# Optimization experiments

Hardware: AMD Instinct MI355X
Metric: run time of the kernel (lower is better)

## Reference

```python
import jax, jax.numpy as jnp
import numpy as np

MASK_LOGIT_CONST = 1000000000.0
LN_EPS = 1e-12


def setup_inputs() -> dict:
    key = jax.random.key(0)
    k_in, k_w = jax.random.split(key)
    B, S, H = 8, 2048, 1024
    inputs = jax.random.normal(k_in, (B, S, H), dtype=jnp.float32)
    masks = jnp.ones((B, S, S), dtype=jnp.float32)
    w_match = jax.random.normal(k_w, (2 * H, H), dtype=jnp.float32) * (1.0 / np.sqrt(2 * H))
    b_match = jnp.zeros((H,), dtype=jnp.float32)
    ln_gamma = jnp.ones((H,), dtype=jnp.float32)
    ln_beta = jnp.zeros((H,), dtype=jnp.float32)
    return {"inputs": inputs, "masks": masks, "w_match": w_match,
            "b_match": b_match, "ln_gamma": ln_gamma, "ln_beta": ln_beta}


def reference(inputs, masks, w_match, b_match, ln_gamma, ln_beta):
    H = inputs.shape[-1]
    scale = 1.0 / jnp.sqrt(jnp.asarray(H, dtype=inputs.dtype))
    # self-attention scores [B,S,S] (dropout disabled -> query=key=inputs)
    scores = jnp.einsum('bsh,bth->bst', inputs, inputs) * scale
    # logits_mask: scores*mask + (-C)*(1-mask)
    scores = scores * masks - MASK_LOGIT_CONST * (1.0 - masks)
    probs = jax.nn.softmax(scores, axis=-1)
    context = jnp.einsum('bst,bth->bsh', probs, inputs)
    cat = jnp.concatenate([inputs, context], axis=-1)  # [B,S,2H]
    matching = jnp.einsum('bsk,kh->bsh', cat, w_match) + b_match
    # layernorm over last dim
    mu = jnp.mean(matching, axis=-1, keepdims=True)
    var = jnp.mean((matching - mu) ** 2, axis=-1, keepdims=True)
    normed = (matching - mu) * jax.lax.rsqrt(var + LN_EPS)
    return normed * ln_gamma + ln_beta
```

## Files before the change

### kernel.cpp

```cpp
#include <hip/hip_runtime.h>
#include <hip/hip_bf16.h>
#include <hip/hip_fp8.h>


typedef unsigned short ushort_t;
typedef __attribute__((ext_vector_type(8))) short short8;
typedef __attribute__((ext_vector_type(4))) float float4v;

__device__ inline float b2f(unsigned int u) {
    union { unsigned int i; float f; } v; v.i = u << 16; return v.f;
}
__device__ inline ushort_t f2b(float f) {
    __hip_bfloat16 h = __float2bfloat16(f);
    return __builtin_bit_cast(ushort_t, h);
}
__device__ inline unsigned char f2e4(float f) {
    return __hip_fp8_e4m3(f).__x;
}

__device__ inline void gload_lds16(const void* g, void* lds) {
    __builtin_amdgcn_global_load_lds(
        (const __attribute__((address_space(1))) unsigned int*)g,
        (__attribute__((address_space(3))) unsigned int*)lds, 16, 0, 0);
}

template<int EPI>
__global__ __launch_bounds__(512, 2)
void gemm_bt(const ushort_t* __restrict__ A, const ushort_t* __restrict__ A2, int kSplit,
             const ushort_t* __restrict__ B,
             int M, int N, int K, int lda, int ldb, int ldc,
             long aBS, long bBS, long cBS,
             const float* __restrict__ rowsum,
             const float* __restrict__ bias,
             ushort_t* __restrict__ outb)
{
    __shared__ __align__(16) ushort_t smem[4 * 16384];

    const int tid = threadIdx.x;
    const int z = blockIdx.z;
    A  += (size_t)z * aBS;
    A2 += (size_t)z * aBS;
    B  += (size_t)z * bBS;
    if (EPI == 2) rowsum += (size_t)z * M;
    outb += (size_t)z * cBS;

    const int bm = blockIdx.x * 256;
    const int bn = blockIdx.y * 256;
    const int w = tid >> 6, lane = tid & 63;
    const int wm = (w >> 2) * 128, wn = (w & 3) * 64;
    const int q = lane >> 4, l15 = lane & 15;
    const int srow = lane >> 2;
    const int schunk = ((lane & 3) ^ ((lane >> 3) & 3)) * 8;

    float4v acc[8][4];
#pragma unroll
    for (int i = 0; i < 8; i++)
#pragma unroll
        for (int j = 0; j < 4; j++) acc[i][j] = (float4v){0.f, 0.f, 0.f, 0.f};

    const int NT = K >> 5;

#define STAGE(T) do {                                                               \
        const int k0_ = (T) * 32;                                                   \
        const ushort_t* aS_ = A; int ka_ = k0_;                                     \
        if (k0_ >= kSplit) { aS_ = A2; ka_ = k0_ - kSplit; }                        \
        ushort_t* buf_ = &smem[((T) & 3) * 16384];                                  \
        gload_lds16(aS_ + (size_t)(bm + w * 16       + srow) * lda + ka_ + schunk,  \
                    buf_ + w * 512);                                                \
        gload_lds16(aS_ + (size_t)(bm + (w + 8) * 16 + srow) * lda + ka_ + schunk,  \
                    buf_ + (w + 8) * 512);                                          \
        gload_lds16(B   + (size_t)(bn + w * 16       + srow) * ldb + k0_ + schunk,  \
                    buf_ + 8192 + w * 512);                                         \
        gload_lds16(B   + (size_t)(bn + (w + 8) * 16 + srow) * ldb + k0_ + schunk,  \
                    buf_ + 8192 + (w + 8) * 512);                                   \
    } while (0)

    STAGE(0); STAGE(1); STAGE(2);

    for (int T = 0; T < NT; ++T) {
        if (T + 2 < NT)      asm volatile("s_waitcnt vmcnt(8)\n\ts_barrier" ::: "memory");
        else if (T + 1 < NT) asm volatile("s_waitcnt vmcnt(4)\n\ts_barrier" ::: "memory");
        else                 asm volatile("s_waitcnt vmcnt(0)\n\ts_barrier" ::: "memory");

        if (T + 3 < NT) STAGE(T + 3);

        const ushort_t* bufA = &smem[(T & 3) * 16384];
        const ushort_t* bufB = bufA + 8192;
        short8 af[8], bf[4];
#pragma unroll
        for (int mi = 0; mi < 8; mi++) {
            const int r = wm + mi * 16 + l15;
            af[mi] = *(const short8*)(&bufA[r * 32 + ((q ^ ((r >> 1) & 3)) << 3)]);
        }
#pragma unroll
        for (int ni = 0; ni < 4; ni++) {
            const int r = wn + ni * 16 + l15;
            bf[ni] = *(const short8*)(&bufB[r * 32 + ((q ^ ((r >> 1) & 3)) << 3)]);
        }
        __builtin_amdgcn_s_setprio(1);
#pragma unroll
        for (int mi = 0; mi < 8; mi++)
#pragma unroll
            for (int ni = 0; ni < 4; ni++)
                acc[mi][ni] = __builtin_amdgcn_mfma_f32_16x16x32_bf16(
                    af[mi], bf[ni], acc[mi][ni], 0, 0, 0);
        __builtin_amdgcn_s_setprio(0);
    }
#undef STAGE

#pragma unroll
    for (int mi = 0; mi < 8; mi++) {
#pragma unroll
        for (int r = 0; r < 4; r++) {
            const int row = bm + wm + mi * 16 + q * 4 + r;
            const size_t ro = (size_t)row * ldc;
            float rsinv = 1.f;
            if (EPI == 2) rsinv = 1.0f / rowsum[row];
#pragma unroll
            for (int ni = 0; ni < 4; ni++) {
                const int col = bn + wn + ni * 16 + l15;
                float v = acc[mi][ni][r];
                if (EPI == 2) outb[ro + col] = f2b(v * rsinv);
                else          outb[ro + col] = f2b(v + bias[col]);
            }
        }
    }
}

__global__ __launch_bounds__(256, 2)
void gemm1_fp8(const unsigned char* __restrict__ X8,
               const float* __restrict__ mask,
               float* __restrict__ rowsum,
               ushort_t* __restrict__ E)
{
    __shared__ __align__(16) unsigned char As[128 * 128];
    __shared__ __align__(16) unsigned char Bs[128 * 128];

    const int tid = threadIdx.x;
    const int z = blockIdx.z;
    const unsigned char* Xz = X8 + (size_t)z * 2048 * 1024;
    const float* mz = mask + (size_t)z * 2048 * 2048;
    float* rsz = rowsum + (size_t)z * 2048;
    ushort_t* Ez = E + (size_t)z * 2048 * 2048;

    const int bm = blockIdx.x * 128;
    const int bn = blockIdx.y * 128;
    const int wave = tid >> 6, lane = tid & 63;
    const int wm = (wave >> 1) * 64, wn = (wave & 1) * 64;
    const int q = lane >> 4, l15 = lane & 15;
    const int rx = l15 & 7;
    const int lrow = lane >> 3;
    const int cswz = (lane & 7) ^ lrow;

    float4v acc[4][4];
#pragma unroll
    for (int i = 0; i < 4; i++)
#pragma unroll
        for (int j = 0; j < 4; j++) acc[i][j] = (float4v){0.f, 0.f, 0.f, 0.f};

    for (int k0 = 0; k0 < 1024; k0 += 128) {
#pragma unroll
        for (int j = 0; j < 4; j++) {
            const int p = wave * 4 + j;
            const int ro = p * 8 + lrow;
            gload_lds16(Xz + (size_t)(bm + ro) * 1024 + k0 + cswz * 16, &As[p * 1024]);
            gload_lds16(Xz + (size_t)(bn + ro) * 1024 + k0 + cswz * 16, &Bs[p * 1024]);
        }
        __syncthreads();
#pragma unroll
        for (int kk = 0; kk < 128; kk += 32) {
            const int g = (kk >> 3) + q;
            const int co = (((g >> 1) ^ rx) << 4) + ((g & 1) << 3);
            long af[4], bfv[4];
#pragma unroll
            for (int mi = 0; mi < 4; mi++)
                af[mi] = *(const long*)(&As[(wm + mi * 16 + l15) * 128 + co]);
#pragma unroll
            for (int ni = 0; ni < 4; ni++)
                bfv[ni] = *(const long*)(&Bs[(wn + ni * 16 + l15) * 128 + co]);
#pragma unroll
            for (int mi = 0; mi < 4; mi++)
#pragma unroll
                for (int ni = 0; ni < 4; ni++)
                    acc[mi][ni] = __builtin_amdgcn_mfma_f32_16x16x32_fp8_fp8(
                        af[mi], bfv[ni], acc[mi][ni], 0, 0, 0);
        }
        __syncthreads();
    }

    const float scale = 0.03125f;
#pragma unroll
    for (int mi = 0; mi < 4; mi++) {
#pragma unroll
        for (int r = 0; r < 4; r++) {
            const int row = bm + wm + mi * 16 + q * 4 + r;
            const size_t ro = (size_t)row * 2048;
            float s = 0.f;
#pragma unroll
            for (int ni = 0; ni < 4; ni++) {
                const int col = bn + wn + ni * 16 + l15;
                const float m = mz[ro + col];
                float v = __expf(acc[mi][ni][r] * scale * m - 1e9f * (1.0f - m));
                s += v;
                Ez[ro + col] = f2b(v);
            }
            s += __shfl_xor(s, 8);
            s += __shfl_xor(s, 4);
            s += __shfl_xor(s, 2);
            s += __shfl_xor(s, 1);
            if (l15 == 0) atomicAdd(&rsz[row], s);
        }
    }
}

__global__ __launch_bounds__(256)
void conv_trans(const float* __restrict__ in, ushort_t* __restrict__ outT,
                ushort_t* __restrict__ outS, unsigned char* __restrict__ outQ,
                int R, int C)
{
    __shared__ float tile[64][65];
    const int tx = threadIdx.x & 15, ty = threadIdx.x >> 4;
    const size_t zoff = (size_t)blockIdx.z * R * C;
    const int r0 = blockIdx.y * 64, c0 = blockIdx.x * 64;
#pragma unroll
    for (int j = 0; j < 4; j++) {
        const int r = ty + j * 16;
        const float4 v = *(const float4*)(in + zoff + (size_t)(r0 + r) * C + c0 + tx * 4);
        tile[r][tx * 4 + 0] = v.x;
        tile[r][tx * 4 + 1] = v.y;
        tile[r][tx * 4 + 2] = v.z;
        tile[r][tx * 4 + 3] = v.w;
        if (outS) {
            ushort4 o;
            o.x = f2b(v.x); o.y = f2b(v.y); o.z = f2b(v.z); o.w = f2b(v.w);
            *(ushort4*)(outS + zoff + (size_t)(r0 + r) * C + c0 + tx * 4) = o;
            uchar4 p;
            p.x = f2e4(v.x); p.y = f2e4(v.y); p.z = f2e4(v.z); p.w = f2e4(v.w);
            *(uchar4*)(outQ + zoff + (size_t)(r0 + r) * C + c0 + tx * 4) = p;
        }
    }
    __syncthreads();
    ushort_t* tp = outT + zoff;
#pragma unroll
    for (int j = 0; j < 4; j++) {
        const int cc = ty + j * 16;
        ushort4 o;
        o.x = f2b(tile[tx * 4 + 0][cc]);
        o.y = f2b(tile[tx * 4 + 1][cc]);
        o.z = f2b(tile[tx * 4 + 2][cc]);
        o.w = f2b(tile[tx * 4 + 3][cc]);
        *(ushort4*)(tp + (size_t)(c0 + cc) * R + r0 + tx * 4) = o;
    }
}

__global__ __launch_bounds__(256)
void ln_k(const ushort_t* __restrict__ Mt, const float* __restrict__ gamma,
          const float* __restrict__ beta, float* __restrict__ out)
{
    const size_t row = blockIdx.x;
    const int tid = threadIdx.x;
    const ushort4 u = *(const ushort4*)(Mt + row * 1024 + tid * 4);
    float x0 = b2f(u.x), x1 = b2f(u.y), x2 = b2f(u.z), x3 = b2f(u.w);
    float s  = x0 + x1 + x2 + x3;
    float s2 = x0 * x0 + x1 * x1 + x2 * x2 + x3 * x3;
#pragma unroll
    for (int off = 32; off > 0; off >>= 1) {
        s  += __shfl_down(s, off);
        s2 += __shfl_down(s2, off);
    }
    __shared__ float red[8];
    const int wave = tid >> 6, lane = tid & 63;
    if (lane == 0) { red[wave] = s; red[4 + wave] = s2; }
    __syncthreads();
    s  = red[0] + red[1] + red[2] + red[3];
    s2 = red[4] + red[5] + red[6] + red[7];
    const float mu  = s * (1.0f / 1024.0f);
    const float var = s2 * (1.0f / 1024.0f) - mu * mu;
    const float rinv = rsqrtf(var + 1e-12f);
    const float4 g = *(const float4*)(gamma + tid * 4);
    const float4 b = *(const float4*)(beta + tid * 4);
    float4 o;
    o.x = (x0 - mu) * rinv * g.x + b.x;
    o.y = (x1 - mu) * rinv * g.y + b.y;
    o.z = (x2 - mu) * rinv * g.z + b.z;
    o.w = (x3 - mu) * rinv * g.w + b.w;
    *(float4*)(out + row * 1024 + tid * 4) = o;
}

extern "C" void kernel_launch(void* const* d_in, const int* in_sizes, int n_in,
                              void* d_out, int out_size, void* d_ws, size_t ws_size,
                              hipStream_t stream)
{
    const float* X     = (const float*)d_in[0];
    const float* masks = (const float*)d_in[1];
    const float* Wm    = (const float*)d_in[2];
    const float* bias  = (const float*)d_in[3];
    const float* gamma = (const float*)d_in[4];
    const float* beta  = (const float*)d_in[5];
    float* out = (float*)d_out;
    char* ws = (char*)d_ws;

    const int B = 8, S = 2048, H = 1024;

    ushort_t* Xb  = (ushort_t*)(ws);
    ushort_t* XT  = (ushort_t*)(ws + 33554432);
    ushort_t* WT  = (ushort_t*)(ws + 67108864);
    ushort_t* E   = (ushort_t*)(ws + 71303168);
    float*    rs  = (float*)   (ws + 138412032);
    ushort_t* CTX = (ushort_t*)(ws + 138477568);
    unsigned char* X8 = (unsigned char*)CTX;
    ushort_t* matching = E;

    conv_trans<<<dim3(16, 32, 8), 256, 0, stream>>>(X, XT, Xb, X8, S, H);
    conv_trans<<<dim3(16, 32, 1), 256, 0, stream>>>(Wm, WT, nullptr, nullptr, 2 * H, H);
    hipMemsetAsync(rs, 0, (size_t)B * S * sizeof(float), stream);

    gemm1_fp8<<<dim3(16, 16, 8), 256, 0, stream>>>(X8, masks, rs, E);

    gemm_bt<2><<<dim3(8, 4, 8), 512, 0, stream>>>(
        E, E, 1 << 30, XT,
        S, H, S, S, S, H,
        (long)S * S, (long)H * S, (long)S * H,
        rs, nullptr, CTX);

    gemm_bt<3><<<dim3(64, 4, 1), 512, 0, stream>>>(
        Xb, CTX, H, WT,
        B * S, H, 2 * H, H, 2 * H, H,
        0, 0, 0,
        nullptr, bias, matching);

    ln_k<<<B * S, 256, 0, stream>>>(matching, gamma, beta, out);
}
```

Measured before the change: 480.8 us.

## Enlarge FP8 score GEMM tile and add four-stage LDS prefetch pipeline

The FP8 QK^T score kernel now computes 256x256 tiles with 8 waves, each owning a 128x64 sub-tile. The K loop uses 64-wide chunks in a 4-buffer LDS ring, keeping three stages in flight through explicit vmcnt waits and a single barrier per step, and raises wave priority around the MFMA block. This aims to hide global-load latency and raise operand reuse per LDS byte. In exchange it uses 128KB of LDS, so likely only one block fits per CU despite the launch bound of 2, and doubles accumulator registers per wave.

```diff
diff --git a/kernel.cpp b/kernel.cpp
--- a/kernel.cpp
+++ b/kernel.cpp
@@ -6,6 +6,7 @@
 typedef unsigned short ushort_t;
 typedef __attribute__((ext_vector_type(8))) short short8;
 typedef __attribute__((ext_vector_type(4))) float float4v;
+typedef __attribute__((ext_vector_type(2))) long long2v;
 
 __device__ inline float b2f(unsigned int u) {
     union { unsigned int i; float f; } v; v.i = u << 16; return v.f;
@@ -127,14 +128,13 @@
     }
 }
 
-__global__ __launch_bounds__(256, 2)
+__global__ __launch_bounds__(512, 2)
 void gemm1_fp8(const unsigned char* __restrict__ X8,
                const float* __restrict__ mask,
                float* __restrict__ rowsum,
                ushort_t* __restrict__ E)
 {
-    __shared__ __align__(16) unsigned char As[128 * 128];
-    __shared__ __align__(16) unsigned char Bs[128 * 128];
+    __shared__ __align__(16) unsigned char smem[4 * 32768];
 
     const int tid = threadIdx.x;
     const int z = blockIdx.z;
@@ -143,54 +143,71 @@
     float* rsz = rowsum + (size_t)z * 2048;
     ushort_t* Ez = E + (size_t)z * 2048 * 2048;
 
-    const int bm = blockIdx.x * 128;
-    const int bn = blockIdx.y * 128;
-    const int wave = tid >> 6, lane = tid & 63;
-    const int wm = (wave >> 1) * 64, wn = (wave & 1) * 64;
+    const int bm = blockIdx.x * 256;
+    const int bn = blockIdx.y * 256;
+    const int w = tid >> 6, lane = tid & 63;
+    const int wm = (w >> 2) * 128, wn = (w & 3) * 64;
     const int q = lane >> 4, l15 = lane & 15;
-    const int rx = l15 & 7;
-    const int lrow = lane >> 3;
-    const int cswz = (lane & 7) ^ lrow;
-
-    float4v acc[4][4];
-#pragma unroll
-    for (int i = 0; i < 4; i++)
+    const int srow = lane >> 2;
+    const int schunk = ((lane & 3) ^ ((lane >> 3) & 3)) * 16;
+
+    float4v acc[8][4];
+#pragma unroll
+    for (int i = 0; i < 8; i++)
 #pragma unroll
         for (int j = 0; j < 4; j++) acc[i][j] = (float4v){0.f, 0.f, 0.f, 0.f};
 
-    for (int k0 = 0; k0 < 1024; k0 += 128) {
-#pragma unroll
-        for (int j = 0; j < 4; j++) {
-            const int p = wave * 4 + j;
-            const int ro = p * 8 + lrow;
-            gload_lds16(Xz + (size_t)(bm + ro) * 1024 + k0 + cswz * 16, &As[p * 1024]);
-            gload_lds16(Xz + (size_t)(bn + ro) * 1024 + k0 + cswz * 16, &Bs[p * 1024]);
-        }
-        __syncthreads();
-#pragma unroll
-        for (int kk = 0; kk < 128; kk += 32) {
-            const int g = (kk >> 3) + q;
-            const int co = (((g >> 1) ^ rx) << 4) + ((g & 1) << 3);
-            long af[4], bfv[4];
-#pragma unroll
-            for (int mi = 0; mi < 4; mi++)
-                af[mi] = *(const long*)(&As[(wm + mi * 16 + l15) * 128 + co]);
-#pragma unroll
-            for (int ni = 0; ni < 4; ni++)
-                bfv[ni] = *(const long*)(&Bs[(wn + ni * 16 + l15) * 128 + co]);
-#pragma unroll
-            for (int mi = 0; mi < 4; mi++)
+#define STAGE1(T) do {                                                                        \
+        const int k0_ = (T) * 64;                                                             \
+        unsigned char* buf_ = &smem[((T) & 3) * 32768];                                       \
+        gload_lds16(Xz + (size_t)(bm + w * 16        + srow) * 1024 + k0_ + schunk,           \
+                    buf_ + w * 1024);                                                         \
+        gload_lds16(Xz + (size_t)(bm + 128 + w * 16  + srow) * 1024 + k0_ + schunk,           \
+                    buf_ + 8192 + w * 1024);                                                  \
+        gload_lds16(Xz + (size_t)(bn + w * 16        + srow) * 1024 + k0_ + schunk,           \
+                    buf_ + 16384 + w * 1024);                                                 \
+        gload_lds16(Xz + (size_t)(bn + 128 + w * 16  + srow) * 1024 + k0_ + schunk,           \
+                    buf_ + 16384 + 8192 + w * 1024);                                          \
+    } while (0)
+
+    STAGE1(0); STAGE1(1); STAGE1(2);
+
+    for (int T = 0; T < 16; ++T) {
+        if (T < 14)      asm volatile("s_waitcnt vmcnt(8)\n\ts_barrier" ::: "memory");
+        else if (T < 15) asm volatile("s_waitcnt vmcnt(4)\n\ts_barrier" ::: "memory");
+        else             asm volatile("s_waitcnt vmcnt(0)\n\ts_barrier" ::: "memory");
+
+        if (T + 3 < 16) STAGE1(T + 3);
+
+        const unsigned char* bufA = &smem[(T & 3) * 32768];
+        const unsigned char* bufB = bufA + 16384;
+        long2v af[8], bf[4];
+#pragma unroll
+        for (int mi = 0; mi < 8; mi++) {
+            const int r = wm + mi * 16 + l15;
+            af[mi] = *(const long2v*)(&bufA[r * 64 + ((q ^ ((r >> 1) & 3)) << 4)]);
+        }
+#pragma unroll
+        for (int ni = 0; ni < 4; ni++) {
+            const int r = wn + ni * 16 + l15;
+            bf[ni] = *(const long2v*)(&bufB[r * 64 + ((q ^ ((r >> 1) & 3)) << 4)]);
+        }
+        __builtin_amdgcn_s_setprio(1);
+#pragma unroll
+        for (int s = 0; s < 2; s++)
+#pragma unroll
+            for (int mi = 0; mi < 8; mi++)
 #pragma unroll
                 for (int ni = 0; ni < 4; ni++)
                     acc[mi][ni] = __builtin_amdgcn_mfma_f32_16x16x32_fp8_fp8(
-                        af[mi], bfv[ni], acc[mi][ni], 0, 0, 0);
-        }
-        __syncthreads();
-    }
+                        af[mi][s], bf[ni][s], acc[mi][ni], 0, 0, 0);
+        __builtin_amdgcn_s_setprio(0);
+    }
+#undef STAGE1
 
     const float scale = 0.03125f;
 #pragma unroll
-    for (int mi = 0; mi < 4; mi++) {
+    for (int mi = 0; mi < 8; mi++) {
 #pragma unroll
         for (int r = 0; r < 4; r++) {
             const int row = bm + wm + mi * 16 + q * 4 + r;
@@ -315,7 +332,7 @@
     conv_trans<<<dim3(16, 32, 1), 256, 0, stream>>>(Wm, WT, nullptr, nullptr, 2 * H, H);
     hipMemsetAsync(rs, 0, (size_t)B * S * sizeof(float), stream);
 
-    gemm1_fp8<<<dim3(16, 16, 8), 256, 0, stream>>>(X8, masks, rs, E);
+    gemm1_fp8<<<dim3(8, 8, 8), 512, 0, stream>>>(X8, masks, rs, E);
 
     gemm_bt<2><<<dim3(8, 4, 8), 512, 0, stream>>>(
         E, E, 1 << 30, XT,
```

Result: slower. 502.4 us (+4.5%).

## Shrink bf16 GEMM tile to 256x128 with double buffering for higher occupancy

Applied to the files above, without the earlier changes.

The shared bf16 GEMM kernel now uses a 256x128 output tile instead of 256x256, and a 2-stage LDS buffer instead of a 4-stage one. Each thread issues 3 async loads per stage, and the wave computes its 128x32 subtile in two halves to keep register use low. Launch bounds rise to 4 blocks per CU and both GEMM launches double their grid in N. The aim is more blocks in flight and better latency hiding on the 256-block grids, at the cost of less data reuse per tile and a shallower prefetch pipeline that waits on all loads every iteration.

```diff
diff --git a/kernel.cpp b/kernel.cpp
--- a/kernel.cpp
+++ b/kernel.cpp
@@ -25,7 +25,7 @@
 }
 
 template<int EPI>
-__global__ __launch_bounds__(512, 2)
+__global__ __launch_bounds__(512, 4)
 void gemm_bt(const ushort_t* __restrict__ A, const ushort_t* __restrict__ A2, int kSplit,
              const ushort_t* __restrict__ B,
              int M, int N, int K, int lda, int ldb, int ldc,
@@ -34,7 +34,7 @@
              const float* __restrict__ bias,
              ushort_t* __restrict__ outb)
 {
-    __shared__ __align__(16) ushort_t smem[4 * 16384];
+    __shared__ __align__(16) ushort_t smem[2 * 12288];
 
     const int tid = threadIdx.x;
     const int z = blockIdx.z;
@@ -45,66 +45,79 @@
     outb += (size_t)z * cBS;
 
     const int bm = blockIdx.x * 256;
-    const int bn = blockIdx.y * 256;
+    const int bn = blockIdx.y * 128;
     const int w = tid >> 6, lane = tid & 63;
-    const int wm = (w >> 2) * 128, wn = (w & 3) * 64;
+    const int wm = (w >> 2) * 128, wn = (w & 3) * 32;
     const int q = lane >> 4, l15 = lane & 15;
-    const int srow = lane >> 2;
-    const int schunk = ((lane & 3) ^ ((lane >> 3) & 3)) * 8;
-
-    float4v acc[8][4];
+    const int srow = tid >> 2;
+    const int schunk = ((tid & 3) ^ ((tid >> 3) & 3)) * 8;
+    const int wbase = w * 512;
+
+    float4v acc[8][2];
 #pragma unroll
     for (int i = 0; i < 8; i++)
 #pragma unroll
-        for (int j = 0; j < 4; j++) acc[i][j] = (float4v){0.f, 0.f, 0.f, 0.f};
+        for (int j = 0; j < 2; j++) acc[i][j] = (float4v){0.f, 0.f, 0.f, 0.f};
 
     const int NT = K >> 5;
 
-#define STAGE(T) do {                                                               \
-        const int k0_ = (T) * 32;                                                   \
-        const ushort_t* aS_ = A; int ka_ = k0_;                                     \
-        if (k0_ >= kSplit) { aS_ = A2; ka_ = k0_ - kSplit; }                        \
-        ushort_t* buf_ = &smem[((T) & 3) * 16384];                                  \
-        gload_lds16(aS_ + (size_t)(bm + w * 16       + srow) * lda + ka_ + schunk,  \
-                    buf_ + w * 512);                                                \
-        gload_lds16(aS_ + (size_t)(bm + (w + 8) * 16 + srow) * lda + ka_ + schunk,  \
-                    buf_ + (w + 8) * 512);                                          \
-        gload_lds16(B   + (size_t)(bn + w * 16       + srow) * ldb + k0_ + schunk,  \
-                    buf_ + 8192 + w * 512);                                         \
-        gload_lds16(B   + (size_t)(bn + (w + 8) * 16 + srow) * ldb + k0_ + schunk,  \
-                    buf_ + 8192 + (w + 8) * 512);                                   \
+#define STAGE(T) do {                                                                \
+        const int k0_ = (T) * 32;                                                    \
+        const ushort_t* aS_ = A; int ka_ = k0_;                                      \
+        if (k0_ >= kSplit) { aS_ = A2; ka_ = k0_ - kSplit; }                         \
+        ushort_t* buf_ = &smem[((T) & 1) * 12288];                                   \
+        gload_lds16(aS_ + (size_t)(bm + srow)       * lda + ka_ + schunk,            \
+                    buf_ + wbase);                                                   \
+        gload_lds16(aS_ + (size_t)(bm + 128 + srow) * lda + ka_ + schunk,            \
+                    buf_ + 4096 + wbase);                                            \
+        gload_lds16(B   + (size_t)(bn + srow)       * ldb + k0_ + schunk,            \
+                    buf_ + 8192 + wbase);                                            \
     } while (0)
 
-    STAGE(0); STAGE(1); STAGE(2);
-
-    for (int T = 0; T < NT; ++T) {
-        if (T + 2 < NT)      asm volatile("s_waitcnt vmcnt(8)\n\ts_barrier" ::: "memory");
-        else if (T + 1 < NT) asm volatile("s_waitcnt vmcnt(4)\n\ts_barrier" ::: "memory");
-        else                 asm volatile("s_waitcnt vmcnt(0)\n\ts_barrier" ::: "memory");
-
-        if (T + 3 < NT) STAGE(T + 3);
-
-        const ushort_t* bufA = &smem[(T & 3) * 16384];
+    STAGE(0);
+    asm volatile("s_waitcnt vmcnt(0)" ::: "memory");
+    __builtin_amdgcn_s_barrier();
+
+    for (int t = 0; t < NT; ++t) {
+        if (t + 1 < NT) STAGE(t + 1);
+
+        const ushort_t* bufA = &smem[(t & 1) * 12288];
         const ushort_t* bufB = bufA + 8192;
-        short8 af[8], bf[4];
-#pragma unroll
-        for (int mi = 0; mi < 8; mi++) {
+        short8 af[4], bf[2];
+#pragma unroll
+        for (int ni = 0; ni < 2; ni++) {
+            const int r = wn + ni * 16 + l15;
+            bf[ni] = *(const short8*)(&bufB[r * 32 + ((q ^ ((r >> 1) & 3)) << 3)]);
+        }
+#pragma unroll
+        for (int mi = 0; mi < 4; mi++) {
             const int r = wm + mi * 16 + l15;
             af[mi] = *(const short8*)(&bufA[r * 32 + ((q ^ ((r >> 1) & 3)) << 3)]);
         }
-#pragma unroll
-        for (int ni = 0; ni < 4; ni++) {
-            const int r = wn + ni * 16 + l15;
-            bf[ni] = *(const short8*)(&bufB[r * 32 + ((q ^ ((r >> 1) & 3)) << 3)]);
-        }
         __builtin_amdgcn_s_setprio(1);
 #pragma unroll
-        for (int mi = 0; mi < 8; mi++)
-#pragma unroll
-            for (int ni = 0; ni < 4; ni++)
+        for (int mi = 0; mi < 4; mi++)
+#pragma unroll
+            for (int ni = 0; ni < 2; ni++)
                 acc[mi][ni] = __builtin_amdgcn_mfma_f32_16x16x32_bf16(
                     af[mi], bf[ni], acc[mi][ni], 0, 0, 0);
         __builtin_amdgcn_s_setprio(0);
+#pragma unroll
+        for (int mi = 0; mi < 4; mi++) {
+            const int r = wm + 64 + mi * 16 + l15;
+            af[mi] = *(const short8*)(&bufA[r * 32 + ((q ^ ((r >> 1) & 3)) << 3)]);
+        }
+        __builtin_amdgcn_s_setprio(1);
+#pragma unroll
+        for (int mi = 0; mi < 4; mi++)
+#pragma unroll
+            for (int ni = 0; ni < 2; ni++)
+                acc[4 + mi][ni] = __builtin_amdgcn_mfma_f32_16x16x32_bf16(
+                    af[mi], bf[ni], acc[4 + mi][ni], 0, 0, 0);
+        __builtin_amdgcn_s_setprio(0);
+
+        asm volatile("s_waitcnt vmcnt(0)" ::: "memory");
+        __builtin_amdgcn_s_barrier();
     }
 #undef STAGE
 
@@ -117,7 +130,7 @@
             float rsinv = 1.f;
             if (EPI == 2) rsinv = 1.0f / rowsum[row];
 #pragma unroll
-            for (int ni = 0; ni < 4; ni++) {
+            for (int ni = 0; ni < 2; ni++) {
                 const int col = bn + wn + ni * 16 + l15;
                 float v = acc[mi][ni][r];
                 if (EPI == 2) outb[ro + col] = f2b(v * rsinv);
@@ -317,13 +330,13 @@
 
     gemm1_fp8<<<dim3(16, 16, 8), 256, 0, stream>>>(X8, masks, rs, E);
 
-    gemm_bt<2><<<dim3(8, 4, 8), 512, 0, stream>>>(
+    gemm_bt<2><<<dim3(8, 8, 8), 512, 0, stream>>>(
         E, E, 1 << 30, XT,
         S, H, S, S, S, H,
         (long)S * S, (long)H * S, (long)S * H,
         rs, nullptr, CTX);
 
-    gemm_bt<3><<<dim3(64, 4, 1), 512, 0, stream>>>(
+    gemm_bt<3><<<dim3(64, 8, 1), 512, 0, stream>>>(
         Xb, CTX, H, WT,
         B * S, H, 2 * H, H, 2 * H, H,
         0, 0, 0,
```

Measured after the change: 500.9 us. 4.2% more time.

## Compute softmax row sums inside PV GEMM and merge conversion launches

Applied to the files above, without the earlier changes.

Softmax denominators are no longer built with atomicAdd in the exp/score kernel. The PV GEMM now sums the bf16 probability fragments it already loads from LDS, reduces them across lanes, and keeps them in shared memory for the normalisation epilogue. This removes the global atomics, the rowsum buffer and its memset. The input and weight transpose/convert kernels are also merged into one launch, using an extra z-slice for the weight. The cost is some extra convert-and-add work inside the GEMM main loop, repeated by every column block.

```diff
diff --git a/kernel.cpp b/kernel.cpp
--- a/kernel.cpp
+++ b/kernel.cpp
@@ -30,7 +30,6 @@
              const ushort_t* __restrict__ B,
              int M, int N, int K, int lda, int ldb, int ldc,
              long aBS, long bBS, long cBS,
-             const float* __restrict__ rowsum,
              const float* __restrict__ bias,
              ushort_t* __restrict__ outb)
 {
@@ -41,7 +40,6 @@
     A  += (size_t)z * aBS;
     A2 += (size_t)z * aBS;
     B  += (size_t)z * bBS;
-    if (EPI == 2) rowsum += (size_t)z * M;
     outb += (size_t)z * cBS;
 
     const int bm = blockIdx.x * 256;
@@ -57,6 +55,8 @@
     for (int i = 0; i < 8; i++)
 #pragma unroll
         for (int j = 0; j < 4; j++) acc[i][j] = (float4v){0.f, 0.f, 0.f, 0.f};
+
+    float rsum0 = 0.f, rsum1 = 0.f;
 
     const int NT = K >> 5;
 
@@ -91,6 +91,12 @@
         for (int mi = 0; mi < 8; mi++) {
             const int r = wm + mi * 16 + l15;
             af[mi] = *(const short8*)(&bufA[r * 32 + ((q ^ ((r >> 1) & 3)) << 3)]);
+            if (EPI == 2 && (mi >> 1) == (w & 3)) {
+                float s8 = 0.f;
+#pragma unroll
+                for (int e = 0; e < 8; e++) s8 += b2f((ushort_t)af[mi][e]);
+                if (mi & 1) rsum1 += s8; else rsum0 += s8;
+            }
         }
 #pragma unroll
         for (int ni = 0; ni < 4; ni++) {
@@ -108,6 +114,18 @@
     }
 #undef STAGE
 
+    float* rsld = (float*)smem;
+    if (EPI == 2) {
+        rsum0 += __shfl_xor(rsum0, 16); rsum0 += __shfl_xor(rsum0, 32);
+        rsum1 += __shfl_xor(rsum1, 16); rsum1 += __shfl_xor(rsum1, 32);
+        if (lane < 16) {
+            const int m0 = 2 * (w & 3);
+            rsld[wm + m0 * 16 + l15]       = rsum0;
+            rsld[wm + (m0 + 1) * 16 + l15] = rsum1;
+        }
+        __syncthreads();
+    }
+
 #pragma unroll
     for (int mi = 0; mi < 8; mi++) {
 #pragma unroll
@@ -115,7 +133,7 @@
             const int row = bm + wm + mi * 16 + q * 4 + r;
             const size_t ro = (size_t)row * ldc;
             float rsinv = 1.f;
-            if (EPI == 2) rsinv = 1.0f / rowsum[row];
+            if (EPI == 2) rsinv = 1.0f / rsld[wm + mi * 16 + q * 4 + r];
 #pragma unroll
             for (int ni = 0; ni < 4; ni++) {
                 const int col = bn + wn + ni * 16 + l15;
@@ -130,7 +148,6 @@
 __global__ __launch_bounds__(256, 2)
 void gemm1_fp8(const unsigned char* __restrict__ X8,
                const float* __restrict__ mask,
-               float* __restrict__ rowsum,
                ushort_t* __restrict__ E)
 {
     __shared__ __align__(16) unsigned char As[128 * 128];
@@ -140,7 +157,6 @@
     const int z = blockIdx.z;
     const unsigned char* Xz = X8 + (size_t)z * 2048 * 1024;
     const float* mz = mask + (size_t)z * 2048 * 2048;
-    float* rsz = rowsum + (size_t)z * 2048;
     ushort_t* Ez = E + (size_t)z * 2048 * 2048;
 
     const int bm = blockIdx.x * 128;
@@ -195,20 +211,13 @@
         for (int r = 0; r < 4; r++) {
             const int row = bm + wm + mi * 16 + q * 4 + r;
             const size_t ro = (size_t)row * 2048;
-            float s = 0.f;
 #pragma unroll
             for (int ni = 0; ni < 4; ni++) {
                 const int col = bn + wn + ni * 16 + l15;
                 const float m = mz[ro + col];
                 float v = __expf(acc[mi][ni][r] * scale * m - 1e9f * (1.0f - m));
-                s += v;
                 Ez[ro + col] = f2b(v);
             }
-            s += __shfl_xor(s, 8);
-            s += __shfl_xor(s, 4);
-            s += __shfl_xor(s, 2);
-            s += __shfl_xor(s, 1);
-            if (l15 == 0) atomicAdd(&rsz[row], s);
         }
     }
 }
@@ -216,31 +225,40 @@
 __global__ __launch_bounds__(256)
 void conv_trans(const float* __restrict__ in, ushort_t* __restrict__ outT,
                 ushort_t* __restrict__ outS, unsigned char* __restrict__ outQ,
+                const float* __restrict__ inW, ushort_t* __restrict__ outTW,
                 int R, int C)
 {
     __shared__ float tile[64][65];
     const int tx = threadIdx.x & 15, ty = threadIdx.x >> 4;
-    const size_t zoff = (size_t)blockIdx.z * R * C;
+    const int z = blockIdx.z;
+    const float* src;
+    ushort_t* dstT; ushort_t* dstS; unsigned char* dstQ;
+    if (z == 8) {
+        src = inW; dstT = outTW; dstS = nullptr; dstQ = nullptr;
+    } else {
+        const size_t zoff = (size_t)z * R * C;
+        src = in + zoff; dstT = outT + zoff;
+        dstS = outS + zoff; dstQ = outQ + zoff;
+    }
     const int r0 = blockIdx.y * 64, c0 = blockIdx.x * 64;
 #pragma unroll
     for (int j = 0; j < 4; j++) {
         const int r = ty + j * 16;
-        const float4 v = *(const float4*)(in + zoff + (size_t)(r0 + r) * C + c0 + tx * 4);
+        const float4 v = *(const float4*)(src + (size_t)(r0 + r) * C + c0 + tx * 4);
         tile[r][tx * 4 + 0] = v.x;
         tile[r][tx * 4 + 1] = v.y;
         tile[r][tx * 4 + 2] = v.z;
         tile[r][tx * 4 + 3] = v.w;
-        if (outS) {
+        if (dstS) {
             ushort4 o;
             o.x = f2b(v.x); o.y = f2b(v.y); o.z = f2b(v.z); o.w = f2b(v.w);
-            *(ushort4*)(outS + zoff + (size_t)(r0 + r) * C + c0 + tx * 4) = o;
+            *(ushort4*)(dstS + (size_t)(r0 + r) * C + c0 + tx * 4) = o;
             uchar4 p;
             p.x = f2e4(v.x); p.y = f2e4(v.y); p.z = f2e4(v.z); p.w = f2e4(v.w);
-            *(uchar4*)(outQ + zoff + (size_t)(r0 + r) * C + c0 + tx * 4) = p;
+            *(uchar4*)(dstQ + (size_t)(r0 + r) * C + c0 + tx * 4) = p;
         }
     }
     __syncthreads();
-    ushort_t* tp = outT + zoff;
 #pragma unroll
     for (int j = 0; j < 4; j++) {
         const int cc = ty + j * 16;
@@ -249,7 +267,7 @@
         o.y = f2b(tile[tx * 4 + 1][cc]);
         o.z = f2b(tile[tx * 4 + 2][cc]);
         o.w = f2b(tile[tx * 4 + 3][cc]);
-        *(ushort4*)(tp + (size_t)(c0 + cc) * R + r0 + tx * 4) = o;
+        *(ushort4*)(dstT + (size_t)(c0 + cc) * R + r0 + tx * 4) = o;
     }
 }
 
@@ -306,28 +324,25 @@
     ushort_t* XT  = (ushort_t*)(ws + 33554432);
     ushort_t* WT  = (ushort_t*)(ws + 67108864);
     ushort_t* E   = (ushort_t*)(ws + 71303168);
-    float*    rs  = (float*)   (ws + 138412032);
     ushort_t* CTX = (ushort_t*)(ws + 138477568);
     unsigned char* X8 = (unsigned char*)CTX;
     ushort_t* matching = E;
 
-    conv_trans<<<dim3(16, 32, 8), 256, 0, stream>>>(X, XT, Xb, X8, S, H);
-    conv_trans<<<dim3(16, 32, 1), 256, 0, stream>>>(Wm, WT, nullptr, nullptr, 2 * H, H);
-    hipMemsetAsync(rs, 0, (size_t)B * S * sizeof(float), stream);
-
-    gemm1_fp8<<<dim3(16, 16, 8), 256, 0, stream>>>(X8, masks, rs, E);
+    conv_trans<<<dim3(16, 32, 9), 256, 0, stream>>>(X, XT, Xb, X8, Wm, WT, S, H);
+
+    gemm1_fp8<<<dim3(16, 16, 8), 256, 0, stream>>>(X8, masks, E);
 
     gemm_bt<2><<<dim3(8, 4, 8), 512, 0, stream>>>(
         E, E, 1 << 30, XT,
         S, H, S, S, S, H,
         (long)S * S, (long)H * S, (long)S * H,
-        rs, nullptr, CTX);
+        nullptr, CTX);
 
     gemm_bt<3><<<dim3(64, 4, 1), 512, 0, stream>>>(
         Xb, CTX, H, WT,
         B * S, H, 2 * H, H, 2 * H, H,
         0, 0, 0,
-        nullptr, bias, matching);
+        bias, matching);
 
     ln_k<<<B * S, 256, 0, stream>>>(matching, gamma, beta, out);
 }
```

New measurement: 473.1 us. About the same (-1.6%).
